# Performance work log

Hardware: AMD Instinct MI355X
Metric: run time of the kernel (lower is better)

The kernel has to match this reference:

```python
import jax, jax.numpy as jnp
import numpy as np

B, CIN, COUT, K, SDIM, H, W = 16, 512, 512, 3, 512, 64, 64


def setup_inputs() -> dict:
    key = jax.random.key(0)
    k1, k2, k3, k4 = jax.random.split(key, 4)
    return {
        "x": jax.random.normal(k1, (B, CIN, H, W), dtype=jnp.float32),
        "style": jax.random.normal(k2, (B, SDIM), dtype=jnp.float32),
        "weight": jax.random.normal(k3, (COUT, CIN, K, K), dtype=jnp.float32),
        "style_w": jax.random.normal(k4, (CIN, SDIM), dtype=jnp.float32),
        "style_b": jnp.ones((CIN,), dtype=jnp.float32),  # bias.data.fill_(1.0)
    }


def reference(x, style, weight, style_w, style_b):
    batch, in_ch, h, w_size = x.shape
    out_ch, _, ks, _ = weight.shape
    pad = ks // 2
    # EqualizedLinear: runtime weight scaling by 1/sqrt(fan_in)
    lin_scale = 1.0 / np.sqrt(style_w.shape[1])
    s = style @ (style_w * lin_scale).T + style_b  # [B, Cin]
    # modulate
    conv_scale = 1.0 / np.sqrt(in_ch * ks * ks)
    wmod = (weight[None] * conv_scale) * s[:, None, :, None, None]  # [B,Cout,Cin,k,k]
    # demodulate
    dcoef = jax.lax.rsqrt(jnp.sum(jnp.square(wmod), axis=(2, 3, 4)) + 1e-8)  # [B,Cout]
    wmod = wmod * dcoef[:, :, None, None, None]
    # grouped conv with groups = batch
    x_r = x.reshape(1, batch * in_ch, h, w_size)
    w_r = wmod.reshape(batch * out_ch, in_ch, ks, ks)
    out = jax.lax.conv_general_dilated(
        x_r, w_r,
        window_strides=(1, 1),
        padding=[(pad, pad), (pad, pad)],
        dimension_numbers=("NCHW", "OIHW", "NCHW"),
        feature_group_count=batch,
    )
    return out.reshape(batch, out_ch, h, w_size)
```

## Files before the change

### kernel.cpp

```cpp
#include <hip/hip_runtime.h>
#include <math.h>

#define B 16
#define CIN 512
#define COUT 512
#define SDIM 512
#define H 64
#define W 64

typedef short s16x8 __attribute__((ext_vector_type(8)));
typedef float f32x4 __attribute__((ext_vector_type(4)));

__device__ __constant__ float LIN_SCALE  = 0.04419417382415922f;
__device__ __constant__ float CONV_SCALE = 0.014731391274719742f;

__device__ __forceinline__ ushort f2bf(float f) {
  unsigned u = __float_as_uint(f);
  return (ushort)((u + 0x7FFFu + ((u >> 16) & 1u)) >> 16);
}

#define GLOAD16(g, l)                                           \
  __builtin_amdgcn_global_load_lds(                             \
      (const __attribute__((address_space(1))) unsigned*)(g),   \
      (__attribute__((address_space(3))) unsigned*)(l), 16, 0, 0)

__global__ __launch_bounds__(512) void style_mod_kernel(
    const float* __restrict__ style, const float* __restrict__ style_w,
    const float* __restrict__ style_b, float* __restrict__ s,
    float* __restrict__ s2) {
  const int b = blockIdx.x;
  const int ci = threadIdx.x;
  __shared__ float st[SDIM];
  st[ci] = style[b * SDIM + ci];
  __syncthreads();

  const float4* wr = reinterpret_cast<const float4*>(style_w + (size_t)ci * SDIM);
  float acc = 0.f;
#pragma unroll 4
  for (int k = 0; k < SDIM / 4; ++k) {
    float4 wv = wr[k];
    acc += st[4 * k + 0] * wv.x + st[4 * k + 1] * wv.y +
           st[4 * k + 2] * wv.z + st[4 * k + 3] * wv.w;
  }
  float v = acc * LIN_SCALE + style_b[ci];
  s[b * CIN + ci] = v;
  s2[b * CIN + ci] = v * v;
}

__global__ __launch_bounds__(256) void wsq_kernel(
    const float* __restrict__ weight, float* __restrict__ wsq) {
  const int i = blockIdx.x * blockDim.x + threadIdx.x;
  if (i >= COUT * CIN) return;
  const float* p = weight + (size_t)i * 9;
  float a = 0.f;
#pragma unroll
  for (int k = 0; k < 9; ++k) {
    float v = p[k];
    a += v * v;
  }
  wsq[i] = a;
}

__global__ __launch_bounds__(512) void dcoef_kernel(
    const float* __restrict__ s2, const float* __restrict__ wsq,
    float* __restrict__ outscale) {
  const int b = blockIdx.x;
  const int co = threadIdx.x;
  __shared__ float sh[CIN];
  sh[co] = s2[b * CIN + co];
  __syncthreads();

  const float4* wr = reinterpret_cast<const float4*>(wsq + (size_t)co * CIN);
  float acc = 0.f;
#pragma unroll 4
  for (int k = 0; k < CIN / 4; ++k) {
    float4 wv = wr[k];
    acc += sh[4 * k + 0] * wv.x + sh[4 * k + 1] * wv.y +
           sh[4 * k + 2] * wv.z + sh[4 * k + 3] * wv.w;
  }
  float d = rsqrtf(acc * CONV_SCALE * CONV_SCALE + 1e-8f);
  outscale[b * COUT + co] = d * CONV_SCALE;
}

__global__ __launch_bounds__(256) void pack_w_kernel(
    const float* __restrict__ w, ushort* __restrict__ wt) {
  const int t = blockIdx.x * 256 + threadIdx.x;
  const int s = t & 3;
  const int chunk = (t >> 2) & 15;
  const int co = t >> 6;
  const float4* wp =
      (const float4*)(w + ((size_t)co * 512 + chunk * 32 + s * 8) * 9);
  float wv[72];
#pragma unroll
  for (int i = 0; i < 18; ++i) {
    float4 v = wp[i];
    wv[4 * i + 0] = v.x; wv[4 * i + 1] = v.y;
    wv[4 * i + 2] = v.z; wv[4 * i + 3] = v.w;
  }
  const int sp = s ^ ((co >> 1) & 3);
  ushort* dst = wt + (size_t)chunk * 147456 + (size_t)co * 32 + sp * 8;
#pragma unroll
  for (int j = 0; j < 9; ++j) {
    s16x8 p;
#pragma unroll
    for (int i = 0; i < 8; ++i) p[i] = (short)f2bf(wv[i * 9 + j]);
    *(s16x8*)(dst + (size_t)j * 16384) = p;
  }
}

__global__ __launch_bounds__(256) void pack_x_kernel(
    const float* __restrict__ x, const float* __restrict__ smod,
    ushort* __restrict__ xp) {
  __shared__ float xt[32][65];
  __shared__ float sm[32];
  const int tid = threadIdx.x;
  const int gr = blockIdx.x, chunk = blockIdx.y, b = blockIdx.z;
  if (tid < 32) sm[tid] = smod[b * 512 + chunk * 32 + tid];
  {
    const int ci = tid >> 3, cq = tid & 7;
    const float4* rp = (const float4*)(
        x + (((size_t)b * 512 + chunk * 32 + ci) * 64 + gr) * 64 + cq * 8);
    float4 a = rp[0], c2 = rp[1];
    float* row = &xt[ci][cq * 8];
    row[0] = a.x; row[1] = a.y; row[2] = a.z; row[3] = a.w;
    row[4] = c2.x; row[5] = c2.y; row[6] = c2.z; row[7] = c2.w;
  }
  __syncthreads();
  const int c = tid >> 2, s = tid & 3;
  s16x8 p;
#pragma unroll
  for (int i = 0; i < 8; ++i)
    p[i] = (short)f2bf(xt[s * 8 + i][c] * sm[s * 8 + i]);
  const int sp = s ^ (((c + 1) >> 1) & 3);
  *(s16x8*)(xp + ((size_t)(b * 16 + chunk) * 64 + gr) * 2048 + c * 32 + sp * 8) = p;
}

#define XS4OFF 36864
#define DLDS4 79104

__global__ __launch_bounds__(256, 2) void conv_mfma4_kernel(
    const ushort* __restrict__ wt, const ushort* __restrict__ xp,
    const float* __restrict__ outscale, float* __restrict__ out) {
  extern __shared__ char smem[];

  const int tid = threadIdx.x;
  const int hb = blockIdx.x;
  const int cb = blockIdx.y;
  const int b  = blockIdx.z;
  const int h0 = hb * 8, co0 = cb * 64;
  const int lane = tid & 63, wid = tid >> 6;
  const int l15 = lane & 15, l4 = lane >> 4;

  {
    s16x8* p = (s16x8*)(smem + XS4OFF);
    for (int e = tid; e < 2640; e += 256) p[e] = (s16x8)0;
  }

  f32x4 acc[2][4][4];
#pragma unroll
  for (int rr = 0; rr < 2; ++rr)
#pragma unroll
    for (int mt = 0; mt < 4; ++mt)
#pragma unroll
      for (int nt = 0; nt < 4; ++nt) acc[rr][mt][nt] = (f32x4)0.f;

  const int am = (l4 ^ ((l15 >> 1) & 3)) * 16;
  int aoff[4];
#pragma unroll
  for (int mt = 0; mt < 4; ++mt) aoff[mt] = (mt * 16 + l15) * 64 + am;
  int bcol[12];
#pragma unroll
  for (int nt = 0; nt < 4; ++nt)
#pragma unroll
    for (int kw = 0; kw < 3; ++kw) {
      int col = nt * 16 + l15 + kw;
      bcol[nt * 3 + kw] = col * 64 + ((l4 ^ ((col >> 1) & 3)) * 16);
    }

  const char* wsrc0 = (const char*)wt + cb * 4096 + tid * 16;
  const char* xsrc0 = (const char*)xp + (size_t)b * 4194304 + tid * 16;
  char* wdst = smem + tid * 16;
  char* xdst = smem + XS4OFF + 64 + tid * 16;
  const char* wb = smem;
  const char* xb = smem + XS4OFF + 2 * wid * 4224;

  __syncthreads();

  for (int chunk = 0; chunk < 16; ++chunk) {
    const char* wsrc = wsrc0 + (size_t)chunk * 294912;
    const char* xsrc = xsrc0 + (size_t)chunk * 262144;
#pragma unroll
    for (int t = 0; t < 9; ++t)
      GLOAD16(wsrc + t * 32768, wdst + t * 4096);
#pragma unroll
    for (int t = 0; t < 10; ++t) {
      int gr = h0 - 1 + t;
      if ((unsigned)gr < 64u)
        GLOAD16(xsrc + (size_t)gr * 4096, xdst + t * 4224);
    }
    __syncthreads();

#pragma unroll
    for (int kh = 0; kh < 3; ++kh) {
#pragma unroll
      for (int kw = 0; kw < 3; ++kw) {
        const int j = kh * 3 + kw;
        const char* wj = wb + j * 4096;
        s16x8 af[4], bf[2][4];
#pragma unroll
        for (int mt = 0; mt < 4; ++mt)
          af[mt] = *(const s16x8*)(wj + aoff[mt]);
#pragma unroll
        for (int rr = 0; rr < 2; ++rr)
#pragma unroll
          for (int nt = 0; nt < 4; ++nt)
            bf[rr][nt] =
                *(const s16x8*)(xb + (rr + kh) * 4224 + bcol[nt * 3 + kw]);
#pragma unroll
        for (int rr = 0; rr < 2; ++rr)
#pragma unroll
          for (int mt = 0; mt < 4; ++mt)
#pragma unroll
            for (int nt = 0; nt < 4; ++nt)
              acc[rr][mt][nt] = __builtin_amdgcn_mfma_f32_16x16x32_bf16(
                  af[mt], bf[rr][nt], acc[rr][mt][nt], 0, 0, 0);
      }
    }
    __syncthreads();
  }

#pragma unroll
  for (int rr = 0; rr < 2; ++rr) {
    const int h = h0 + 2 * wid + rr;
#pragma unroll
    for (int mt = 0; mt < 4; ++mt) {
#pragma unroll
      for (int r = 0; r < 4; ++r) {
        const int co = co0 + mt * 16 + l4 * 4 + r;
        const float osc = outscale[b * COUT + co];
        float* orow = out + (((size_t)b * COUT + co) * H + h) * W;
#pragma unroll
        for (int nt = 0; nt < 4; ++nt)
          orow[nt * 16 + l15] = acc[rr][mt][nt][r] * osc;
      }
    }
  }
}

__global__ __launch_bounds__(256, 2) void conv_mfma2_kernel(
    const ushort* __restrict__ wt, const ushort* __restrict__ xp,
    const float* __restrict__ outscale, float* __restrict__ out) {
  __shared__ ushort ws[9][64][32];
  __shared__ ushort xs[6][66][32];

  const int tid = threadIdx.x;
  const int hb = blockIdx.x, cb = blockIdx.y, b = blockIdx.z;
  const int h0 = hb * 4, co0 = cb * 64;
  const int lane = tid & 63, wid = tid >> 6;
  const int l15 = lane & 15, l4 = lane >> 4;

  {
    s16x8* p = (s16x8*)&xs[0][0][0];
    for (int e = tid; e < 1584; e += 256) p[e] = (s16x8)0;
  }

  f32x4 acc[4][4];
#pragma unroll
  for (int mt = 0; mt < 4; ++mt)
#pragma unroll
    for (int nt = 0; nt < 4; ++nt) acc[mt][nt] = (f32x4)0.f;

  const int am = (l4 ^ ((l15 >> 1) & 3)) * 16;
  int aoff[4];
#pragma unroll
  for (int mt = 0; mt < 4; ++mt) aoff[mt] = (mt * 16 + l15) * 64 + am;
  int boff[12];
#pragma unroll
  for (int nt = 0; nt < 4; ++nt)
#pragma unroll
    for (int kw = 0; kw < 3; ++kw) {
      int col = nt * 16 + l15 + kw;
      boff[nt * 3 + kw] =
          wid * 4224 + col * 64 + ((l4 ^ ((col >> 1) & 3)) * 16);
    }

  const char* wsrc0 = (const char*)wt + cb * 4096 + wid * 1024 + lane * 16;
  const char* xsrc0 =
      (const char*)xp + (size_t)b * 4194304 + wid * 1024 + lane * 16;
  char* wdst = (char*)&ws[0][0][0] + wid * 1024 + lane * 16;
  char* xdst = (char*)&xs[0][0][0] + 64 + wid * 1024 + lane * 16;

  __syncthreads();

  for (int chunk = 0; chunk < 16; ++chunk) {
    const char* wsrc = wsrc0 + chunk * 294912;
    const char* xsrc = xsrc0 + chunk * 262144;
#pragma unroll
    for (int t = 0; t < 9; ++t)
      GLOAD16(wsrc + t * 32768, wdst + t * 4096);
#pragma unroll
    for (int t = 0; t < 6; ++t) {
      int gr = h0 - 1 + t;
      if ((unsigned)gr < 64u) GLOAD16(xsrc + gr * 4096, xdst + t * 4224);
    }
    __syncthreads();

#pragma unroll
    for (int kh = 0; kh < 3; ++kh) {
      const char* xrow = (const char*)&xs[0][0][0] + kh * 4224;
#pragma unroll
      for (int kw = 0; kw < 3; ++kw) {
        const int j = kh * 3 + kw;
        const char* wj = (const char*)&ws[0][0][0] + j * 4096;
        s16x8 af[4], bf[4];
#pragma unroll
        for (int mt = 0; mt < 4; ++mt)
          af[mt] = *(const s16x8*)(wj + aoff[mt]);
#pragma unroll
        for (int nt = 0; nt < 4; ++nt)
          bf[nt] = *(const s16x8*)(xrow + boff[nt * 3 + kw]);
#pragma unroll
        for (int mt = 0; mt < 4; ++mt)
#pragma unroll
          for (int nt = 0; nt < 4; ++nt)
            acc[mt][nt] = __builtin_amdgcn_mfma_f32_16x16x32_bf16(
                af[mt], bf[nt], acc[mt][nt], 0, 0, 0);
      }
    }
    __syncthreads();
  }

  const int h = h0 + wid;
#pragma unroll
  for (int mt = 0; mt < 4; ++mt) {
#pragma unroll
    for (int r = 0; r < 4; ++r) {
      const int co = co0 + mt * 16 + l4 * 4 + r;
      const float osc = outscale[b * COUT + co];
      float* orow = out + (((size_t)b * COUT + co) * H + h) * W;
#pragma unroll
      for (int nt = 0; nt < 4; ++nt)
        orow[nt * 16 + l15] = acc[mt][nt][r] * osc;
    }
  }
}

extern "C" void kernel_launch(void* const* d_in, const int* in_sizes, int n_in,
                              void* d_out, int out_size, void* d_ws,
                              size_t ws_size, hipStream_t stream) {
  const float* x = (const float*)d_in[0];
  const float* style = (const float*)d_in[1];
  const float* weight = (const float*)d_in[2];
  const float* style_w = (const float*)d_in[3];
  const float* style_b = (const float*)d_in[4];
  float* out = (float*)d_out;

  char* wsb = (char*)d_ws;
  float* s = (float*)(wsb + 0);
  float* s2 = (float*)(wsb + 32768);
  float* wsq = (float*)(wsb + 65536);
  float* outscale = (float*)(wsb + 1114112);
  ushort* wt = (ushort*)(wsb + 1146880);
  ushort* xp = (ushort*)(wsb + 5865472);
  const size_t NEED = 72974336;

  style_mod_kernel<<<B, 512, 0, stream>>>(style, style_w, style_b, s, s2);
  wsq_kernel<<<(COUT * CIN + 255) / 256, 256, 0, stream>>>(weight, wsq);
  dcoef_kernel<<<B, 512, 0, stream>>>(s2, wsq, outscale);

  pack_w_kernel<<<128, 256, 0, stream>>>(weight, wt);
  pack_x_kernel<<<dim3(64, 16, 16), 256, 0, stream>>>(x, s, xp);

  hipError_t attr_ok = hipFuncSetAttribute(
      reinterpret_cast<const void*>(conv_mfma4_kernel),
      hipFuncAttributeMaxDynamicSharedMemorySize, DLDS4);

  if (attr_ok == hipSuccess && ws_size >= NEED) {
    conv_mfma4_kernel<<<dim3(8, 8, 16), 256, DLDS4, stream>>>(wt, xp, outscale,
                                                              out);
  } else {
    conv_mfma2_kernel<<<dim3(16, 8, 16), 256, 0, stream>>>(wt, xp, outscale,
                                                           out);
  }
}
```

Baseline: 340.7 us.

## Switch conv inner loop to 32x32x16 MFMA with kw-outer B-fragment reuse

Replaces the 16x16x32 bf16 MFMA tiling with 32x32x16 bf16 MFMA, giving each wave 2x2 tiles of 32x32 per output row. The loop is reordered so the input fragments for all four needed rows are loaded once per kw and reused across the three kh taps. The goal is fewer LDS reads per MFMA and a larger instruction granularity. In exchange the output store pattern and register layout change, the kernel holds more live B fragments, and register pressure may rise.

```diff
diff --git a/kernel.cpp b/kernel.cpp
--- a/kernel.cpp
+++ b/kernel.cpp
@@ -10,6 +10,7 @@
 
 typedef short s16x8 __attribute__((ext_vector_type(8)));
 typedef float f32x4 __attribute__((ext_vector_type(4)));
+typedef float f32x16 __attribute__((ext_vector_type(16)));
 
 __device__ __constant__ float LIN_SCALE  = 0.04419417382415922f;
 __device__ __constant__ float CONV_SCALE = 0.014731391274719742f;
@@ -138,7 +139,7 @@
 #define XS4OFF 36864
 #define DLDS4 79104
 
-__global__ __launch_bounds__(256, 2) void conv_mfma4_kernel(
+__global__ __launch_bounds__(256, 2) void conv_mfma5_kernel(
     const ushort* __restrict__ wt, const ushort* __restrict__ xp,
     const float* __restrict__ outscale, float* __restrict__ out) {
   extern __shared__ char smem[];
@@ -149,33 +150,39 @@
   const int b  = blockIdx.z;
   const int h0 = hb * 8, co0 = cb * 64;
   const int lane = tid & 63, wid = tid >> 6;
-  const int l15 = lane & 15, l4 = lane >> 4;
+  const int l31 = lane & 31, hi = lane >> 5;
 
   {
     s16x8* p = (s16x8*)(smem + XS4OFF);
     for (int e = tid; e < 2640; e += 256) p[e] = (s16x8)0;
   }
 
-  f32x4 acc[2][4][4];
+  f32x16 acc[2][2][2];
 #pragma unroll
   for (int rr = 0; rr < 2; ++rr)
 #pragma unroll
-    for (int mt = 0; mt < 4; ++mt)
-#pragma unroll
-      for (int nt = 0; nt < 4; ++nt) acc[rr][mt][nt] = (f32x4)0.f;
-
-  const int am = (l4 ^ ((l15 >> 1) & 3)) * 16;
-  int aoff[4];
-#pragma unroll
-  for (int mt = 0; mt < 4; ++mt) aoff[mt] = (mt * 16 + l15) * 64 + am;
-  int bcol[12];
-#pragma unroll
-  for (int nt = 0; nt < 4; ++nt)
-#pragma unroll
-    for (int kw = 0; kw < 3; ++kw) {
-      int col = nt * 16 + l15 + kw;
-      bcol[nt * 3 + kw] = col * 64 + ((l4 ^ ((col >> 1) & 3)) * 16);
-    }
+    for (int mt = 0; mt < 2; ++mt)
+#pragma unroll
+      for (int nt = 0; nt < 2; ++nt) acc[rr][mt][nt] = (f32x16)0.f;
+
+  const int akey = (l31 >> 1) & 3;
+  int aoff[2][2];
+#pragma unroll
+  for (int mt = 0; mt < 2; ++mt)
+#pragma unroll
+    for (int ks = 0; ks < 2; ++ks)
+      aoff[mt][ks] = (mt * 32 + l31) * 64 + ((ks * 2 + hi) ^ akey) * 16;
+
+  int boff[3][2][2];
+#pragma unroll
+  for (int kw = 0; kw < 3; ++kw)
+#pragma unroll
+    for (int nt = 0; nt < 2; ++nt)
+#pragma unroll
+      for (int ks = 0; ks < 2; ++ks) {
+        int cc = nt * 32 + l31 + kw;
+        boff[kw][nt][ks] = cc * 64 + (((ks * 2 + hi) ^ ((cc >> 1) & 3))) * 16;
+      }
 
   const char* wsrc0 = (const char*)wt + cb * 4096 + tid * 16;
   const char* xsrc0 = (const char*)xp + (size_t)b * 4194304 + tid * 16;
@@ -201,47 +208,52 @@
     __syncthreads();
 
 #pragma unroll
-    for (int kh = 0; kh < 3; ++kh) {
-#pragma unroll
-      for (int kw = 0; kw < 3; ++kw) {
-        const int j = kh * 3 + kw;
-        const char* wj = wb + j * 4096;
-        s16x8 af[4], bf[2][4];
-#pragma unroll
-        for (int mt = 0; mt < 4; ++mt)
-          af[mt] = *(const s16x8*)(wj + aoff[mt]);
-#pragma unroll
-        for (int rr = 0; rr < 2; ++rr)
-#pragma unroll
-          for (int nt = 0; nt < 4; ++nt)
-            bf[rr][nt] =
-                *(const s16x8*)(xb + (rr + kh) * 4224 + bcol[nt * 3 + kw]);
-#pragma unroll
-        for (int rr = 0; rr < 2; ++rr)
-#pragma unroll
-          for (int mt = 0; mt < 4; ++mt)
-#pragma unroll
-            for (int nt = 0; nt < 4; ++nt)
-              acc[rr][mt][nt] = __builtin_amdgcn_mfma_f32_16x16x32_bf16(
-                  af[mt], bf[rr][nt], acc[rr][mt][nt], 0, 0, 0);
+    for (int kw = 0; kw < 3; ++kw) {
+      s16x8 bf[4][2][2];
+#pragma unroll
+      for (int q = 0; q < 4; ++q)
+#pragma unroll
+        for (int nt = 0; nt < 2; ++nt)
+#pragma unroll
+          for (int ks = 0; ks < 2; ++ks)
+            bf[q][nt][ks] =
+                *(const s16x8*)(xb + q * 4224 + boff[kw][nt][ks]);
+#pragma unroll
+      for (int kh = 0; kh < 3; ++kh) {
+        const char* wj = wb + (kh * 3 + kw) * 4096;
+#pragma unroll
+        for (int ks = 0; ks < 2; ++ks) {
+          s16x8 af0 = *(const s16x8*)(wj + aoff[0][ks]);
+          s16x8 af1 = *(const s16x8*)(wj + aoff[1][ks]);
+#pragma unroll
+          for (int rr = 0; rr < 2; ++rr)
+#pragma unroll
+            for (int nt = 0; nt < 2; ++nt) {
+              acc[rr][0][nt] = __builtin_amdgcn_mfma_f32_32x32x16_bf16(
+                  af0, bf[rr + kh][nt][ks], acc[rr][0][nt], 0, 0, 0);
+              acc[rr][1][nt] = __builtin_amdgcn_mfma_f32_32x32x16_bf16(
+                  af1, bf[rr + kh][nt][ks], acc[rr][1][nt], 0, 0, 0);
+            }
+        }
       }
     }
     __syncthreads();
   }
 
 #pragma unroll
-  for (int rr = 0; rr < 2; ++rr) {
-    const int h = h0 + 2 * wid + rr;
-#pragma unroll
-    for (int mt = 0; mt < 4; ++mt) {
-#pragma unroll
-      for (int r = 0; r < 4; ++r) {
-        const int co = co0 + mt * 16 + l4 * 4 + r;
-        const float osc = outscale[b * COUT + co];
-        float* orow = out + (((size_t)b * COUT + co) * H + h) * W;
-#pragma unroll
-        for (int nt = 0; nt < 4; ++nt)
-          orow[nt * 16 + l15] = acc[rr][mt][nt][r] * osc;
+  for (int mt = 0; mt < 2; ++mt) {
+#pragma unroll
+    for (int reg = 0; reg < 16; ++reg) {
+      const int row = (reg & 3) + 8 * (reg >> 2) + 4 * hi;
+      const int co = co0 + mt * 32 + row;
+      const float osc = outscale[b * COUT + co];
+      float* obase = out + ((size_t)b * COUT + co) * H * W;
+#pragma unroll
+      for (int rr = 0; rr < 2; ++rr) {
+        const int h = h0 + 2 * wid + rr;
+#pragma unroll
+        for (int nt = 0; nt < 2; ++nt)
+          obase[h * W + nt * 32 + l31] = acc[rr][mt][nt][reg] * osc;
       }
     }
   }
@@ -372,11 +384,11 @@
   pack_x_kernel<<<dim3(64, 16, 16), 256, 0, stream>>>(x, s, xp);
 
   hipError_t attr_ok = hipFuncSetAttribute(
-      reinterpret_cast<const void*>(conv_mfma4_kernel),
+      reinterpret_cast<const void*>(conv_mfma5_kernel),
       hipFuncAttributeMaxDynamicSharedMemorySize, DLDS4);
 
   if (attr_ok == hipSuccess && ws_size >= NEED) {
-    conv_mfma4_kernel<<<dim3(8, 8, 16), 256, DLDS4, stream>>>(wt, xp, outscale,
+    conv_mfma5_kernel<<<dim3(8, 8, 16), 256, DLDS4, stream>>>(wt, xp, outscale,
                                                               out);
   } else {
     conv_mfma2_kernel<<<dim3(16, 8, 16), 256, 0, stream>>>(wt, xp, outscale,
```

Result: slower. 347.9 us (+2.1%).
